# Kernel optimization log

Hardware: AMD Instinct MI355X
Metric: run time of the kernel (lower is better)

The kernel has to match this reference:

```python
import jax, jax.numpy as jnp
import numpy as np

H, KVH, HD, HID = 16, 8, 128, 2048
GROUPS = H // KVH
THETA = 10000.0
EPS = 1e-6


def _rms_norm(x, w):
    # x: (..., HD), norm in fp32 like Qwen3RMSNorm
    xf = x.astype(jnp.float32)
    var = jnp.mean(xf * xf, axis=-1, keepdims=True)
    return (xf * jax.lax.rsqrt(var + EPS)).astype(x.dtype) * w


def _rope_cos_sin(position_ids, dtype):
    # position_ids: (B, S) int
    inv_freq = 1.0 / (THETA ** (jnp.arange(0, HD, 2, dtype=jnp.float32) / HD))  # (HD/2,)
    freqs = position_ids.astype(jnp.float32)[..., None] * inv_freq  # (B, S, HD/2)
    emb = jnp.concatenate([freqs, freqs], axis=-1)  # (B, S, HD)
    return jnp.cos(emb).astype(dtype), jnp.sin(emb).astype(dtype)


def _rotate_half(x):
    x1, x2 = jnp.split(x, 2, axis=-1)
    return jnp.concatenate([-x2, x1], axis=-1)


def _apply_rope(q, k, cos, sin):
    # q,k: (B, h, S, HD); cos,sin: (B, S, HD) -> broadcast over head dim
    cos = cos[:, None, :, :]
    sin = sin[:, None, :, :]
    q = q * cos + _rotate_half(q) * sin
    k = k * cos + _rotate_half(k) * sin
    return q, k


def setup_inputs() -> dict:
    key = jax.random.key(0)
    ks = jax.random.split(key, 10)
    B, S, L = 1, 2048, 2048
    w = 0.02
    return {
        "hidden_states": jax.random.normal(ks[0], (B, S, HID), jnp.float32),
        "context": jax.random.normal(ks[1], (B, L, HID), jnp.float32),
        "position_ids": jnp.arange(S, dtype=jnp.int64)[None, :].repeat(B, axis=0),
        "Wq": jax.random.normal(ks[2], (H * HD, HID), jnp.float32) * w,
        "Wk": jax.random.normal(ks[3], (KVH * HD, HID), jnp.float32) * w,
        "Wv": jax.random.normal(ks[4], (KVH * HD, HID), jnp.float32) * w,
        "Wo": jax.random.normal(ks[5], (HID, H * HD), jnp.float32) * w,
        "Wk_ctx": jax.random.normal(ks[6], (KVH * HD, HID), jnp.float32) * w,
        "Wv_ctx": jax.random.normal(ks[7], (KVH * HD, HID), jnp.float32) * w,
        "q_norm_w": jnp.ones((HD,), jnp.float32),
        "k_norm_w": jnp.ones((HD,), jnp.float32),
    }


def reference(hidden_states, context, position_ids, Wq, Wk, Wv, Wo, Wk_ctx, Wv_ctx, q_norm_w, k_norm_w):
    B, S, _ = hidden_states.shape
    L = context.shape[1]
    scaling = HD ** -0.5

    Q = (hidden_states @ Wq.T).reshape(B, S, H, HD).transpose(0, 2, 1, 3)    # (B,H,S,HD)
    K = (hidden_states @ Wk.T).reshape(B, S, KVH, HD).transpose(0, 2, 1, 3)  # (B,KVH,S,HD)
    V = (hidden_states @ Wv.T).reshape(B, S, KVH, HD).transpose(0, 2, 1, 3)

    Q = _rms_norm(Q, q_norm_w)
    K = _rms_norm(K, k_norm_w)

    cos, sin = _rope_cos_sin(position_ids, Q.dtype)
    Q, K = _apply_rope(Q, K, cos, sin)

    K_ctx = (context @ Wk_ctx.T).reshape(B, L, KVH, HD).transpose(0, 2, 1, 3)
    V_ctx = (context @ Wv_ctx.T).reshape(B, L, KVH, HD).transpose(0, 2, 1, 3)

    K_full = jnp.concatenate([K_ctx, K], axis=2)  # (B,KVH,L+S,HD)
    V_full = jnp.concatenate([V_ctx, V], axis=2)
    K_full = jnp.repeat(K_full, GROUPS, axis=1)   # (B,H,L+S,HD)
    V_full = jnp.repeat(V_full, GROUPS, axis=1)

    attn = jnp.einsum("bhsd,bhtd->bhst", Q, K_full) * scaling  # (B,H,S,L+S)
    attn = jax.nn.softmax(attn.astype(jnp.float32), axis=-1).astype(Q.dtype)
    out = jnp.einsum("bhst,bhtd->bhsd", attn, V_full)          # (B,H,S,HD)
    out = out.transpose(0, 2, 1, 3).reshape(B, S, H * HD)
    return out @ Wo.T
```

## Files before the change

kernel.cpp:

```cpp
#include <hip/hip_runtime.h>

typedef __bf16 bf16_t;
typedef __attribute__((ext_vector_type(8))) __bf16 bf16x8;
typedef __attribute__((ext_vector_type(4))) __bf16 bf16x4;
typedef __attribute__((ext_vector_type(4))) float f32x4;

#define LDA_PAD 72
#define LDK_PAD 136
#define LDV_PAD 72
#define LDP_PAD 72

__device__ __forceinline__ bf16x8 ld8(const float* g) {
  f32x4 a = *(const f32x4*)g;
  f32x4 b = *(const f32x4*)(g + 4);
  bf16x8 r;
  r[0] = (bf16_t)a[0]; r[1] = (bf16_t)a[1]; r[2] = (bf16_t)a[2]; r[3] = (bf16_t)a[3];
  r[4] = (bf16_t)b[0]; r[5] = (bf16_t)b[1]; r[6] = (bf16_t)b[2]; r[7] = (bf16_t)b[3];
  return r;
}
__device__ __forceinline__ bf16x8 ld8(const bf16_t* g) { return *(const bf16x8*)g; }

struct CvtArgs { const float* src[8]; bf16_t* dst[8]; };

__global__ __launch_bounds__(256) void cvt_all(CvtArgs a) {
  const int g = blockIdx.x * 256 + threadIdx.x;
  int seg, base;
  if (g < 1048576)      { if (g < 524288)  { seg = 0; base = 0; }
                          else             { seg = 1; base = 524288; } }
  else if (g < 2097152) { if (g < 1572864) { seg = 2; base = 1048576; }
                          else if (g < 1835008) { seg = 3; base = 1572864; }
                          else             { seg = 4; base = 1835008; } }
  else                  { if (g < 2359296) { seg = 5; base = 2097152; }
                          else if (g < 2621440) { seg = 6; base = 2359296; }
                          else             { seg = 7; base = 2621440; } }
  const size_t off = (size_t)(g - base) * 8;
  *(bf16x8*)(a.dst[seg] + off) = ld8(a.src[seg] + off);
}

template<typename TI>
__global__ __launch_bounds__(256) void proj_all(
    const TI* __restrict__ hs, const TI* __restrict__ ctx,
    const TI* __restrict__ Wq, const TI* __restrict__ Wk,
    const TI* __restrict__ Wv, const TI* __restrict__ Wkc,
    const TI* __restrict__ Wvc,
    bf16_t* __restrict__ Qb, bf16_t* __restrict__ Kb, bf16_t* __restrict__ Vt)
{
  __shared__ __align__(16) bf16_t lA[128 * LDA_PAD];
  __shared__ __align__(16) bf16_t lB[128 * LDA_PAD];
  const int tid = threadIdx.x, wave = tid >> 6, lane = tid & 63;
  const int quad = lane >> 4, lc = lane & 15;
  const int u = blockIdx.x;
  const int xcd = u & 7, v = u >> 3;
  const int op = v >> 5, w = v & 31;
  const int nh = w >> 4, mt0 = w & 15;
  const int n0 = (xcd + nh * 8) * 128, m0 = mt0 * 128;
  const TI* A; const TI* B;
  if (op == 0) { A = hs; B = Wq + (size_t)n0 * 2048; }
  else {
    A = (op == 1) ? ctx : hs;
    const TI* WK = (op == 1) ? Wkc : Wk;
    const TI* WV = (op == 1) ? Wvc : Wv;
    B = (n0 < 1024) ? WK + (size_t)n0 * 2048 : WV + (size_t)(n0 - 1024) * 2048;
  }
  const int mw = (wave >> 1) * 64, nw = (wave & 1) * 64;
  const int lr8 = lane >> 3, lc8 = (lane & 7) * 8;

  f32x4 acc[4][4];
#pragma unroll
  for (int i = 0; i < 4; ++i)
#pragma unroll
    for (int j = 0; j < 4; ++j) acc[i][j] = (f32x4){0.f, 0.f, 0.f, 0.f};

  bf16x8 pa[4], pb[4];
#pragma unroll
  for (int i = 0; i < 4; ++i) {
    const int row = (wave + 4 * i) * 8 + lr8;
    pa[i] = ld8(A + (size_t)(m0 + row) * 2048 + lc8);
    pb[i] = ld8(B + (size_t)row * 2048 + lc8);
  }

  for (int k0 = 0; k0 < 2048; k0 += 64) {
    __syncthreads();
#pragma unroll
    for (int i = 0; i < 4; ++i) {
      const int row = (wave + 4 * i) * 8 + lr8;
      *(bf16x8*)(lA + row * LDA_PAD + lc8) = pa[i];
      *(bf16x8*)(lB + row * LDA_PAD + lc8) = pb[i];
    }
    __syncthreads();
    if (k0 + 64 < 2048) {
      const int kn = k0 + 64;
#pragma unroll
      for (int i = 0; i < 4; ++i) {
        const int row = (wave + 4 * i) * 8 + lr8;
        pa[i] = ld8(A + (size_t)(m0 + row) * 2048 + kn + lc8);
        pb[i] = ld8(B + (size_t)row * 2048 + kn + lc8);
      }
    }
#pragma unroll
    for (int kk = 0; kk < 2; ++kk) {
      bf16x8 af[4], bfv[4];
#pragma unroll
      for (int mt = 0; mt < 4; ++mt)
        af[mt] = *(const bf16x8*)(lA + (mw + mt * 16 + lc) * LDA_PAD + kk * 32 + quad * 8);
#pragma unroll
      for (int nt = 0; nt < 4; ++nt)
        bfv[nt] = *(const bf16x8*)(lB + (nw + nt * 16 + lc) * LDA_PAD + kk * 32 + quad * 8);
#pragma unroll
      for (int mt = 0; mt < 4; ++mt)
#pragma unroll
        for (int nt = 0; nt < 4; ++nt)
          acc[mt][nt] = __builtin_amdgcn_mfma_f32_16x16x32_bf16(af[mt], bfv[nt], acc[mt][nt], 0, 0, 0);
    }
  }

  if (op == 0) {
#pragma unroll
    for (int mt = 0; mt < 4; ++mt)
#pragma unroll
      for (int nt = 0; nt < 4; ++nt)
#pragma unroll
        for (int r = 0; r < 4; ++r)
          Qb[(size_t)(m0 + mw + mt * 16 + quad * 4 + r) * 2048 + n0 + nw + nt * 16 + lc]
              = (bf16_t)acc[mt][nt][r];
  } else {
    const int t_off = (op == 1) ? 0 : 2048;
    if (n0 < 1024) {
#pragma unroll
      for (int mt = 0; mt < 4; ++mt)
#pragma unroll
        for (int nt = 0; nt < 4; ++nt)
#pragma unroll
          for (int r = 0; r < 4; ++r) {
            const int n = n0 + nw + nt * 16 + lc;
            const int kvh = n >> 7, dd = n & 127;
            const int t = t_off + m0 + mw + mt * 16 + quad * 4 + r;
            Kb[((size_t)kvh * 4096 + t) * 128 + dd] = (bf16_t)acc[mt][nt][r];
          }
    } else {
#pragma unroll
      for (int mt = 0; mt < 4; ++mt)
#pragma unroll
        for (int nt = 0; nt < 4; ++nt) {
          const int n = n0 - 1024 + nw + nt * 16 + lc;
          const int kvh = n >> 7, dd = n & 127;
          const int t = t_off + m0 + mw + mt * 16 + quad * 4;
          bf16x4 pk;
#pragma unroll
          for (int r = 0; r < 4; ++r) pk[r] = (bf16_t)acc[mt][nt][r];
          *(bf16x4*)(Vt + ((size_t)kvh * 128 + dd) * 4096 + t) = pk;
        }
    }
  }
}

__global__ __launch_bounds__(256) void normrope(
    bf16_t* __restrict__ Q, bf16_t* __restrict__ Kb,
    const float* __restrict__ qw, const float* __restrict__ kw)
{
  const int wave = threadIdx.x >> 6, lane = threadIdx.x & 63;
  const int row = blockIdx.x * 4 + wave;
  bf16_t* p; const float* w; int pos;
  if (row < 32768) {
    const int s = row >> 4, hh = row & 15;
    p = Q + (size_t)s * 2048 + hh * 128; w = qw; pos = s;
  } else {
    const int rk = row - 32768;
    const int s = rk >> 3, hh = rk & 7;
    p = Kb + ((size_t)hh * 4096 + 2048 + s) * 128; w = kw; pos = s;
  }
  const float x1 = (float)p[lane], x2 = (float)p[lane + 64];
  float ss = x1 * x1 + x2 * x2;
#pragma unroll
  for (int m = 1; m < 64; m <<= 1) ss += __shfl_xor(ss, m, 64);
  const float inv = rsqrtf(ss * (1.0f / 128.0f) + 1e-6f);
  const float y1 = x1 * inv * w[lane];
  const float y2 = x2 * inv * w[lane + 64];
  const float freq = (float)pos * exp2f((float)lane * (-13.287712379549449f / 64.0f));
  const float cb = cosf(freq), sb = sinf(freq);
  p[lane]      = (bf16_t)(y1 * cb - y2 * sb);
  p[lane + 64] = (bf16_t)(y2 * cb + y1 * sb);
}

__global__ __launch_bounds__(256) void attn_kernel(
    const bf16_t* __restrict__ Q, const bf16_t* __restrict__ Kb,
    const bf16_t* __restrict__ Vt, bf16_t* __restrict__ O)
{
  __shared__ __align__(16) bf16_t lK[64 * LDK_PAD];
  __shared__ __align__(16) bf16_t lV[128 * LDV_PAD];
  __shared__ __align__(16) bf16_t lP[4 * 16 * LDP_PAD];
  const int tid = threadIdx.x, wave = tid >> 6, lane = tid & 63;
  const int quad = lane >> 4, lc = lane & 15;
  const int bid = blockIdx.x;
  const int hk = bid & 7, qt = (bid >> 3) & 31, hsel = bid >> 8;
  const int h = hk * 2 + hsel;
  const int mrow0 = qt * 64 + wave * 16;
  const float cexp = 0.08838834764831845f * 1.4426950408889634f;

  bf16x8 qf[4];
  {
    const bf16_t* qb = Q + (size_t)(mrow0 + lc) * 2048 + h * 128 + quad * 8;
#pragma unroll
    for (int ks = 0; ks < 4; ++ks) qf[ks] = *(const bf16x8*)(qb + ks * 32);
  }
  float rs[4] = {0.f, 0.f, 0.f, 0.f};
  f32x4 oacc[8];
#pragma unroll
  for (int ot = 0; ot < 8; ++ot) oacc[ot] = (f32x4){0.f, 0.f, 0.f, 0.f};

  bf16x8 kp[4], vp[4];
  auto load_tile = [&](int t0) {
    const bf16_t* Kt = Kb + ((size_t)hk * 4096 + t0) * 128;
    const bf16_t* Vb = Vt + (size_t)hk * 524288 + t0;
#pragma unroll
    for (int i = 0; i < 4; ++i) {
      const int g = wave + 4 * i;
      kp[i] = *(const bf16x8*)(Kt + (size_t)(g * 4 + quad) * 128 + lc * 8);
      vp[i] = *(const bf16x8*)(Vb + (size_t)(g * 8 + (lane >> 3)) * 4096 + (lane & 7) * 8);
    }
  };
  load_tile(0);

  for (int t0 = 0; t0 < 4096; t0 += 64) {
    __syncthreads();
#pragma unroll
    for (int i = 0; i < 4; ++i) {
      const int g = wave + 4 * i;
      *(bf16x8*)(lK + (g * 4 + quad) * LDK_PAD + lc * 8) = kp[i];
      *(bf16x8*)(lV + (g * 8 + (lane >> 3)) * LDV_PAD + (lane & 7) * 8) = vp[i];
    }
    __syncthreads();
    if (t0 + 64 < 4096) load_tile(t0 + 64);

    f32x4 s[4];
#pragma unroll
    for (int nt = 0; nt < 4; ++nt) {
      f32x4 a = (f32x4){0.f, 0.f, 0.f, 0.f};
#pragma unroll
      for (int ks = 0; ks < 4; ++ks) {
        bf16x8 kf = *(const bf16x8*)(lK + (nt * 16 + lc) * LDK_PAD + ks * 32 + quad * 8);
        a = __builtin_amdgcn_mfma_f32_16x16x32_bf16(qf[ks], kf, a, 0, 0, 0);
      }
      s[nt] = a;
    }

#pragma unroll
    for (int nt = 0; nt < 4; ++nt)
#pragma unroll
      for (int r = 0; r < 4; ++r) {
        const float pv = exp2f(s[nt][r] * cexp);
        rs[r] += pv;
        lP[wave * (16 * LDP_PAD) + (quad * 4 + r) * LDP_PAD + nt * 16 + lc] = (bf16_t)pv;
      }

#pragma unroll
    for (int ks2 = 0; ks2 < 2; ++ks2) {
      bf16x8 pf = *(const bf16x8*)(lP + wave * (16 * LDP_PAD) + lc * LDP_PAD + ks2 * 32 + quad * 8);
#pragma unroll
      for (int ot = 0; ot < 8; ++ot) {
        bf16x8 vf = *(const bf16x8*)(lV + (ot * 16 + lc) * LDV_PAD + ks2 * 32 + quad * 8);
        oacc[ot] = __builtin_amdgcn_mfma_f32_16x16x32_bf16(pf, vf, oacc[ot], 0, 0, 0);
      }
    }
  }

  float l_r[4];
#pragma unroll
  for (int r = 0; r < 4; ++r) {
    float vv = rs[r];
    vv += __shfl_xor(vv, 1, 64);
    vv += __shfl_xor(vv, 2, 64);
    vv += __shfl_xor(vv, 4, 64);
    vv += __shfl_xor(vv, 8, 64);
    l_r[r] = vv;
  }
#pragma unroll
  for (int ot = 0; ot < 8; ++ot)
#pragma unroll
    for (int r = 0; r < 4; ++r)
      O[(size_t)(mrow0 + quad * 4 + r) * 2048 + h * 128 + ot * 16 + lc]
          = (bf16_t)(oacc[ot][r] / l_r[r]);
}

template<typename TB>
__global__ __launch_bounds__(256) void gemm_o(
    const bf16_t* __restrict__ A, const TB* __restrict__ Bw,
    float* __restrict__ C)
{
  __shared__ __align__(16) bf16_t lA[128 * LDA_PAD];
  __shared__ __align__(16) bf16_t lB[64 * LDA_PAD];
  const int tid = threadIdx.x, wave = tid >> 6, lane = tid & 63;
  const int quad = lane >> 4, lc = lane & 15;
  const int bid = blockIdx.x;
  const int xcd = bid & 7, v = bid >> 3;
  const int nh = v >> 4, mt0 = v & 15;
  const int n0 = (xcd + nh * 8) * 64, m0 = mt0 * 128;
  const int mw = (wave >> 1) * 64, nw = (wave & 1) * 32;
  const int lr8 = lane >> 3, lc8 = (lane & 7) * 8;

  f32x4 acc[4][2];
#pragma unroll
  for (int i = 0; i < 4; ++i)
#pragma unroll
    for (int j = 0; j < 2; ++j) acc[i][j] = (f32x4){0.f, 0.f, 0.f, 0.f};

  bf16x8 pa[4], pb[2];
#pragma unroll
  for (int i = 0; i < 4; ++i)
    pa[i] = ld8(A + (size_t)(m0 + (wave + 4 * i) * 8 + lr8) * 2048 + lc8);
#pragma unroll
  for (int i = 0; i < 2; ++i)
    pb[i] = ld8(Bw + (size_t)(n0 + i * 32 + wave * 8 + lr8) * 2048 + lc8);

  for (int k0 = 0; k0 < 2048; k0 += 64) {
    __syncthreads();
#pragma unroll
    for (int i = 0; i < 4; ++i)
      *(bf16x8*)(lA + ((wave + 4 * i) * 8 + lr8) * LDA_PAD + lc8) = pa[i];
#pragma unroll
    for (int i = 0; i < 2; ++i)
      *(bf16x8*)(lB + (i * 32 + wave * 8 + lr8) * LDA_PAD + lc8) = pb[i];
    __syncthreads();
    if (k0 + 64 < 2048) {
      const int kn = k0 + 64;
#pragma unroll
      for (int i = 0; i < 4; ++i)
        pa[i] = ld8(A + (size_t)(m0 + (wave + 4 * i) * 8 + lr8) * 2048 + kn + lc8);
#pragma unroll
      for (int i = 0; i < 2; ++i)
        pb[i] = ld8(Bw + (size_t)(n0 + i * 32 + wave * 8 + lr8) * 2048 + kn + lc8);
    }
#pragma unroll
    for (int kk = 0; kk < 2; ++kk) {
      bf16x8 af[4], bfv[2];
#pragma unroll
      for (int mt = 0; mt < 4; ++mt)
        af[mt] = *(const bf16x8*)(lA + (mw + mt * 16 + lc) * LDA_PAD + kk * 32 + quad * 8);
#pragma unroll
      for (int nt = 0; nt < 2; ++nt)
        bfv[nt] = *(const bf16x8*)(lB + (nw + nt * 16 + lc) * LDA_PAD + kk * 32 + quad * 8);
#pragma unroll
      for (int mt = 0; mt < 4; ++mt)
#pragma unroll
        for (int nt = 0; nt < 2; ++nt)
          acc[mt][nt] = __builtin_amdgcn_mfma_f32_16x16x32_bf16(af[mt], bfv[nt], acc[mt][nt], 0, 0, 0);
    }
  }
#pragma unroll
  for (int mt = 0; mt < 4; ++mt)
#pragma unroll
    for (int nt = 0; nt < 2; ++nt)
#pragma unroll
      for (int r = 0; r < 4; ++r)
        C[(size_t)(m0 + mw + mt * 16 + quad * 4 + r) * 2048 + n0 + nw + nt * 16 + lc]
            = acc[mt][nt][r];
}

extern "C" void kernel_launch(void* const* d_in, const int* in_sizes, int n_in,
                              void* d_out, int out_size, void* d_ws, size_t ws_size,
                              hipStream_t stream)
{
  const float* hs  = (const float*)d_in[0];
  const float* ctx = (const float*)d_in[1];
  const float* Wq  = (const float*)d_in[3];
  const float* Wk  = (const float*)d_in[4];
  const float* Wv  = (const float*)d_in[5];
  const float* Wo  = (const float*)d_in[6];
  const float* Wkc = (const float*)d_in[7];
  const float* Wvc = (const float*)d_in[8];
  const float* qw  = (const float*)d_in[9];
  const float* kw  = (const float*)d_in[10];

  bf16_t* Kb = (bf16_t*)d_out;
  bf16_t* Vt = Kb + (size_t)4 * 1024 * 1024;
  bf16_t* wsb = (bf16_t*)d_ws;
  const bool fast = ws_size >= (size_t)64 * 1024 * 1024;

  dim3 blk(256);
  if (fast) {
    bf16_t* hs_b  = wsb;
    bf16_t* ctx_b = wsb + (size_t)8  * 524288;
    bf16_t* Wq_b  = wsb + (size_t)16 * 524288;
    bf16_t* Wk_b  = wsb + (size_t)24 * 524288;
    bf16_t* Wv_b  = wsb + (size_t)28 * 524288;
    bf16_t* Wkc_b = wsb + (size_t)32 * 524288;
    bf16_t* Wvc_b = wsb + (size_t)36 * 524288;
    bf16_t* Wo_b  = wsb + (size_t)40 * 524288;
    bf16_t* Qb    = wsb + (size_t)48 * 524288;
    bf16_t* Ob    = wsb + (size_t)56 * 524288;
    CvtArgs ca;
    ca.src[0] = hs;  ca.dst[0] = hs_b;
    ca.src[1] = ctx; ca.dst[1] = ctx_b;
    ca.src[2] = Wq;  ca.dst[2] = Wq_b;
    ca.src[3] = Wk;  ca.dst[3] = Wk_b;
    ca.src[4] = Wv;  ca.dst[4] = Wv_b;
    ca.src[5] = Wkc; ca.dst[5] = Wkc_b;
    ca.src[6] = Wvc; ca.dst[6] = Wvc_b;
    ca.src[7] = Wo;  ca.dst[7] = Wo_b;
    cvt_all<<<dim3(12288), blk, 0, stream>>>(ca);
    proj_all<bf16_t><<<dim3(768), blk, 0, stream>>>(
        hs_b, ctx_b, Wq_b, Wk_b, Wv_b, Wkc_b, Wvc_b, Qb, Kb, Vt);
    normrope<<<dim3(12288), blk, 0, stream>>>(Qb, Kb, qw, kw);
    attn_kernel<<<dim3(512), blk, 0, stream>>>(Qb, Kb, Vt, Ob);
    gemm_o<bf16_t><<<dim3(512), blk, 0, stream>>>(Ob, Wo_b, (float*)d_out);
  } else {
    bf16_t* Qb = wsb;
    bf16_t* Ob = wsb + (size_t)8 * 524288;
    proj_all<float><<<dim3(768), blk, 0, stream>>>(
        hs, ctx, Wq, Wk, Wv, Wkc, Wvc, Qb, Kb, Vt);
    normrope<<<dim3(12288), blk, 0, stream>>>(Qb, Kb, qw, kw);
    attn_kernel<<<dim3(512), blk, 0, stream>>>(Qb, Kb, Vt, Ob);
    gemm_o<float><<<dim3(512), blk, 0, stream>>>(Ob, Wo, (float*)d_out);
  }
}
```

Before: 377.1 us.

## Split attention over KV halves with combine kernel and swizzled LDS

Attention is split into two halves along the key length, doubling the block count. Each half writes unnormalized fp32 partial outputs and row sums, and a new combine kernel merges them into bf16. LDS padding is replaced with XOR swizzling, and MFMA sections get raised wave priority along with a 4-blocks occupancy hint. This aims to fill the GPU better, at the cost of extra fp32 global traffic and an additional launch.

```diff
diff --git a/kernel.cpp b/kernel.cpp
--- a/kernel.cpp
+++ b/kernel.cpp
@@ -6,9 +6,6 @@
 typedef __attribute__((ext_vector_type(4))) float f32x4;
 
 #define LDA_PAD 72
-#define LDK_PAD 136
-#define LDV_PAD 72
-#define LDP_PAD 72
 
 __device__ __forceinline__ bf16x8 ld8(const float* g) {
   f32x4 a = *(const f32x4*)g;
@@ -182,19 +179,24 @@
   p[lane + 64] = (bf16_t)(y2 * cb + y1 * sb);
 }
 
-__global__ __launch_bounds__(256) void attn_kernel(
+template<int SPLIT>
+__global__ __launch_bounds__(256, 4) void attn_kernel(
     const bf16_t* __restrict__ Q, const bf16_t* __restrict__ Kb,
-    const bf16_t* __restrict__ Vt, bf16_t* __restrict__ O)
-{
-  __shared__ __align__(16) bf16_t lK[64 * LDK_PAD];
-  __shared__ __align__(16) bf16_t lV[128 * LDV_PAD];
-  __shared__ __align__(16) bf16_t lP[4 * 16 * LDP_PAD];
+    const bf16_t* __restrict__ Vt, bf16_t* __restrict__ O,
+    float* __restrict__ Of, float* __restrict__ Lf)
+{
+  __shared__ __align__(16) char lK[64 * 256];
+  __shared__ __align__(16) char lV[128 * 128];
+  __shared__ __align__(16) char lP[4 * 2048];
   const int tid = threadIdx.x, wave = tid >> 6, lane = tid & 63;
   const int quad = lane >> 4, lc = lane & 15;
   const int bid = blockIdx.x;
-  const int hk = bid & 7, qt = (bid >> 3) & 31, hsel = bid >> 8;
+  const int hk = bid & 7, qt = (bid >> 3) & 31, hsel = (bid >> 8) & 1;
+  const int half = SPLIT ? (bid >> 9) : 0;
   const int h = hk * 2 + hsel;
   const int mrow0 = qt * 64 + wave * 16;
+  const int tbase = half * 2048;
+  const int tend = tbase + (SPLIT ? 2048 : 4096);
   const float cexp = 0.08838834764831845f * 1.4426950408889634f;
 
   bf16x8 qf[4];
@@ -219,30 +221,37 @@
       vp[i] = *(const bf16x8*)(Vb + (size_t)(g * 8 + (lane >> 3)) * 4096 + (lane & 7) * 8);
     }
   };
-  load_tile(0);
-
-  for (int t0 = 0; t0 < 4096; t0 += 64) {
+  load_tile(tbase);
+
+  char* lPw = lP + wave * 2048;
+  const int sw_rd = (lc & 7) << 4;
+
+  for (int t0 = tbase; t0 < tend; t0 += 64) {
     __syncthreads();
 #pragma unroll
     for (int i = 0; i < 4; ++i) {
       const int g = wave + 4 * i;
-      *(bf16x8*)(lK + (g * 4 + quad) * LDK_PAD + lc * 8) = kp[i];
-      *(bf16x8*)(lV + (g * 8 + (lane >> 3)) * LDV_PAD + (lane & 7) * 8) = vp[i];
-    }
-    __syncthreads();
-    if (t0 + 64 < 4096) load_tile(t0 + 64);
+      const int kr = g * 4 + quad;
+      *(bf16x8*)(lK + kr * 256 + ((lc * 16) ^ ((kr & 7) << 4))) = kp[i];
+      const int vr = g * 8 + (lane >> 3);
+      *(bf16x8*)(lV + vr * 128 + (((lane & 7) * 16) ^ ((vr & 7) << 4))) = vp[i];
+    }
+    __syncthreads();
+    if (t0 + 64 < tend) load_tile(t0 + 64);
 
     f32x4 s[4];
+    __builtin_amdgcn_s_setprio(1);
 #pragma unroll
     for (int nt = 0; nt < 4; ++nt) {
       f32x4 a = (f32x4){0.f, 0.f, 0.f, 0.f};
 #pragma unroll
       for (int ks = 0; ks < 4; ++ks) {
-        bf16x8 kf = *(const bf16x8*)(lK + (nt * 16 + lc) * LDK_PAD + ks * 32 + quad * 8);
+        bf16x8 kf = *(const bf16x8*)(lK + (nt * 16 + lc) * 256 + ((ks * 64 + quad * 16) ^ sw_rd));
         a = __builtin_amdgcn_mfma_f32_16x16x32_bf16(qf[ks], kf, a, 0, 0, 0);
       }
       s[nt] = a;
     }
+    __builtin_amdgcn_s_setprio(0);
 
 #pragma unroll
     for (int nt = 0; nt < 4; ++nt)
@@ -250,18 +259,21 @@
       for (int r = 0; r < 4; ++r) {
         const float pv = exp2f(s[nt][r] * cexp);
         rs[r] += pv;
-        lP[wave * (16 * LDP_PAD) + (quad * 4 + r) * LDP_PAD + nt * 16 + lc] = (bf16_t)pv;
+        const int pr = quad * 4 + r;
+        *(bf16_t*)(lPw + pr * 128 + ((nt * 32 + lc * 2) ^ ((pr & 7) << 4))) = (bf16_t)pv;
       }
 
+    __builtin_amdgcn_s_setprio(1);
 #pragma unroll
     for (int ks2 = 0; ks2 < 2; ++ks2) {
-      bf16x8 pf = *(const bf16x8*)(lP + wave * (16 * LDP_PAD) + lc * LDP_PAD + ks2 * 32 + quad * 8);
+      bf16x8 pf = *(const bf16x8*)(lPw + lc * 128 + ((ks2 * 64 + quad * 16) ^ sw_rd));
 #pragma unroll
       for (int ot = 0; ot < 8; ++ot) {
-        bf16x8 vf = *(const bf16x8*)(lV + (ot * 16 + lc) * LDV_PAD + ks2 * 32 + quad * 8);
+        bf16x8 vf = *(const bf16x8*)(lV + (ot * 16 + lc) * 128 + ((ks2 * 64 + quad * 16) ^ sw_rd));
         oacc[ot] = __builtin_amdgcn_mfma_f32_16x16x32_bf16(pf, vf, oacc[ot], 0, 0, 0);
       }
     }
+    __builtin_amdgcn_s_setprio(0);
   }
 
   float l_r[4];
@@ -274,12 +286,51 @@
     vv += __shfl_xor(vv, 8, 64);
     l_r[r] = vv;
   }
-#pragma unroll
-  for (int ot = 0; ot < 8; ++ot)
-#pragma unroll
-    for (int r = 0; r < 4; ++r)
-      O[(size_t)(mrow0 + quad * 4 + r) * 2048 + h * 128 + ot * 16 + lc]
-          = (bf16_t)(oacc[ot][r] / l_r[r]);
+  if (SPLIT) {
+    float* Oh = Of + (size_t)half * 4194304;
+#pragma unroll
+    for (int ot = 0; ot < 8; ++ot)
+#pragma unroll
+      for (int r = 0; r < 4; ++r)
+        Oh[(size_t)(mrow0 + quad * 4 + r) * 2048 + h * 128 + ot * 16 + lc] = oacc[ot][r];
+    if (lc == 0) {
+      float* Lh = Lf + half * 32768 + h * 2048 + mrow0;
+#pragma unroll
+      for (int r = 0; r < 4; ++r) Lh[quad * 4 + r] = l_r[r];
+    }
+  } else {
+#pragma unroll
+    for (int ot = 0; ot < 8; ++ot)
+#pragma unroll
+      for (int r = 0; r < 4; ++r)
+        O[(size_t)(mrow0 + quad * 4 + r) * 2048 + h * 128 + ot * 16 + lc]
+            = (bf16_t)(oacc[ot][r] / l_r[r]);
+  }
+}
+
+__global__ __launch_bounds__(256) void combine(
+    const float* __restrict__ Of, const float* __restrict__ Lf,
+    bf16_t* __restrict__ Ob)
+{
+  const int b = blockIdx.x;
+  const int hk = b & 7, idx = b >> 3;
+  const int h = hk * 2 + (idx & 1), sg = idx >> 1;
+  const int t = threadIdx.x;
+  const int s = sg * 16 + (t >> 4), d = (t & 15) * 8;
+  const size_t e = (size_t)s * 2048 + h * 128 + d;
+  const float l = Lf[h * 2048 + s] + Lf[32768 + h * 2048 + s];
+  const float inv = 1.0f / l;
+  f32x4 a0 = *(const f32x4*)(Of + e);
+  f32x4 a1 = *(const f32x4*)(Of + e + 4);
+  f32x4 b0 = *(const f32x4*)(Of + 4194304 + e);
+  f32x4 b1 = *(const f32x4*)(Of + 4194304 + e + 4);
+  bf16x8 rr;
+#pragma unroll
+  for (int j = 0; j < 4; ++j) {
+    rr[j]     = (bf16_t)((a0[j] + b0[j]) * inv);
+    rr[4 + j] = (bf16_t)((a1[j] + b1[j]) * inv);
+  }
+  *(bf16x8*)(Ob + e) = rr;
 }
 
 template<typename TB>
@@ -388,6 +439,8 @@
     bf16_t* Wo_b  = wsb + (size_t)40 * 524288;
     bf16_t* Qb    = wsb + (size_t)48 * 524288;
     bf16_t* Ob    = wsb + (size_t)56 * 524288;
+    float*  Of    = (float*)wsb;
+    float*  Lfp   = (float*)(wsb + (size_t)16 * 1024 * 1024);
     CvtArgs ca;
     ca.src[0] = hs;  ca.dst[0] = hs_b;
     ca.src[1] = ctx; ca.dst[1] = ctx_b;
@@ -401,7 +454,8 @@
     proj_all<bf16_t><<<dim3(768), blk, 0, stream>>>(
         hs_b, ctx_b, Wq_b, Wk_b, Wv_b, Wkc_b, Wvc_b, Qb, Kb, Vt);
     normrope<<<dim3(12288), blk, 0, stream>>>(Qb, Kb, qw, kw);
-    attn_kernel<<<dim3(512), blk, 0, stream>>>(Qb, Kb, Vt, Ob);
+    attn_kernel<1><<<dim3(1024), blk, 0, stream>>>(Qb, Kb, Vt, nullptr, Of, Lfp);
+    combine<<<dim3(2048), blk, 0, stream>>>(Of, Lfp, Ob);
     gemm_o<bf16_t><<<dim3(512), blk, 0, stream>>>(Ob, Wo_b, (float*)d_out);
   } else {
     bf16_t* Qb = wsb;
@@ -409,7 +463,7 @@
     proj_all<float><<<dim3(768), blk, 0, stream>>>(
         hs, ctx, Wq, Wk, Wv, Wkc, Wvc, Qb, Kb, Vt);
     normrope<<<dim3(12288), blk, 0, stream>>>(Qb, Kb, qw, kw);
-    attn_kernel<<<dim3(512), blk, 0, stream>>>(Qb, Kb, Vt, Ob);
+    attn_kernel<0><<<dim3(512), blk, 0, stream>>>(Qb, Kb, Vt, Ob, nullptr, nullptr);
     gemm_o<float><<<dim3(512), blk, 0, stream>>>(Ob, Wo, (float*)d_out);
   }
 }
```

New measurement: 505.8 us. +34.1%, slower.
